# Performance work log

Measured on AMD Instinct MI355X. Metric: run time of the kernel, lower is better.

## Reference

```python
import jax, jax.numpy as jnp
import numpy as np

BATCH = 128
N = 4096
STEPNUM = 100
X = 10.0
DX = X / N               # grid spacing
BETA = 0.1
DT = 0.75 * DX / 1.5     # CFL-stable dt per module's update() rule (max|f'| ~ 1.5)


def _flux(u):
    # f_real with is_real=True:
    # f = 0.5*u*(3 - u^2) + beta/12 * u^2 * (3/4 - 2u + 3/2 u^2 - 1/4 u^4)
    u2 = u * u
    return 0.5 * u * (3.0 - u2) + (BETA / 12.0) * u2 * (0.75 - 2.0 * u + 1.5 * u2 - 0.25 * u2 * u2)


def _dflux(u):
    # analytic df/du (same value torch.autograd.grad computes in df_du)
    u2 = u * u
    u3 = u2 * u
    return 1.5 - 1.5 * u2 + (BETA / 12.0) * (1.5 * u - 6.0 * u2 + 6.0 * u3 - 1.5 * u2 * u3)


def setup_inputs() -> dict:
    key = jax.random.key(0)
    init = jax.random.uniform(key, (BATCH, N), dtype=jnp.float32)  # [B, N] in [0,1)
    return {"init": init, "stepnum": STEPNUM}


def reference(init, stepnum):
    r = jnp.float32(DT / DX)

    def step(u, _):
        f = _flux(u)                       # [B, N]
        a = jnp.abs(_dflux(u))             # [B, N], |f'(u)|
        # local Lax-Friedrichs speed: max over each adjacent pair (== torch.max over 2-slice)
        amax = jnp.maximum(a[:, :-1], a[:, 1:])                     # [B, N-1]
        f_half = 0.5 * (f[:, :-1] + f[:, 1:]) - 0.5 * amax * (u[:, 1:] - u[:, :-1])
        interior = u[:, 1:-1] - r * (f_half[:, 1:] - f_half[:, :-1])  # [B, N-2]
        # boundary copy: u[:,0]=u[:,1], u[:,N-1]=u[:,N-2]
        u_new = jnp.concatenate([interior[:, :1], interior, interior[:, -1:]], axis=1)
        return u_new, u_new

    _, traj = jax.lax.scan(step, init, None, length=stepnum - 1)  # [stepnum-1, B, N]
    return jnp.concatenate([init[None], traj], axis=0)           # [stepnum, B, N]
```

## Files before the change

### kernel.cpp

```cpp
#include <hip/hip_runtime.h>

#define BATCH 128
#define NPTS  4096
#define EPT   8
#define WREG  (64 * EPT)
#define HALOC 104
#define OWN   (WREG - 2 * HALOC)
#define SEGS  14
#define TPB   64

__device__ __forceinline__ void flux_eval(float u, float& g, float& ah) {
    constexpr float b  = 0.1f / 12.0f;
    constexpr float c6 = 0.5f * (-0.25f * b);
    constexpr float c4 = 0.5f * ( 1.5f  * b);
    constexpr float c3 = 0.5f * (-0.5f - 2.0f * b);
    constexpr float c2 = 0.5f * ( 0.75f * b);
    constexpr float c1 = 0.5f * ( 1.5f);
    constexpr float d5 = 0.5f * (-1.5f * b);
    constexpr float d3 = 0.5f * ( 6.0f * b);
    constexpr float d2 = 0.5f * (-(1.5f + 6.0f * b));
    constexpr float d1 = 0.5f * ( 1.5f * b);
    constexpr float d0 = 0.5f * ( 1.5f);

    float t = c6 * u;
    t = fmaf(t, u, c4);
    t = fmaf(t, u, c3);
    t = fmaf(t, u, c2);
    t = fmaf(t, u, c1);
    g = u * t;

    float e = d5 * u;
    e = fmaf(e, u, d3);
    e = fmaf(e, u, d2);
    e = fmaf(e, u, d1);
    e = fmaf(e, u, d0);
    ah = fabsf(e);
}

__global__ __launch_bounds__(TPB) void pde_wave_indep(
        const float* __restrict__ init,
        const int*   __restrict__ stepnum_p,
        float*       __restrict__ out) {
    const int wid  = blockIdx.x;
    const int lane = threadIdx.x;
    const int row  = wid / SEGS;
    const int seg  = wid - row * SEGS;

    const int ownlo = seg * OWN;
    const int base  = min(max(ownlo - HALOC, 0), NPTS - WREG);
    const int c0    = base + lane * EPT;
    const bool ownstore = (c0 >= ownlo) && (c0 < ownlo + OWN) && (c0 < NPTS);
    const bool bcL = (seg == 0) && (lane == 0);
    const bool bcR = (seg == SEGS - 1) && (lane == 63);
    const int stepnum = *stepnum_p;

    const float* ip = init + (size_t)row * NPTS + c0;
    const float4 A  = *(const float4*)ip;
    const float4 Bv = *(const float4*)(ip + 4);
    float v[EPT] = {A.x, A.y, A.z, A.w, Bv.x, Bv.y, Bv.z, Bv.w};

    float* op = out + (size_t)row * NPTS + c0;
    const size_t zstride = (size_t)BATCH * NPTS;

    if (ownstore) {
        *(float4*)op       = A;
        *(float4*)(op + 4) = Bv;
    }

    for (int s = 1; s < stepnum; ++s) {
        const float vl = __shfl_up(v[EPT - 1], 1, 64);
        const float vr = __shfl_down(v[0], 1, 64);

        float vv[EPT + 2];
        vv[0] = vl;
#pragma unroll
        for (int i = 0; i < EPT; ++i) vv[i + 1] = v[i];
        vv[EPT + 1] = vr;

        float g[EPT + 2], a[EPT + 2];
#pragma unroll
        for (int i = 0; i < EPT + 2; ++i) flux_eval(vv[i], g[i], a[i]);

        float fh[EPT + 1];
#pragma unroll
        for (int m = 0; m < EPT + 1; ++m)
            fh[m] = g[m] + g[m + 1] - fmaxf(a[m], a[m + 1]) * (vv[m + 1] - vv[m]);

#pragma unroll
        for (int i = 0; i < EPT; ++i)
            v[i] = fmaf(-0.5f, fh[i + 1] - fh[i], v[i]);

        if (bcL) v[0] = v[1];
        if (bcR) v[EPT - 1] = v[EPT - 2];

        op += zstride;
        if (ownstore) {
            *(float4*)op       = make_float4(v[0], v[1], v[2], v[3]);
            *(float4*)(op + 4) = make_float4(v[4], v[5], v[6], v[7]);
        }
    }
}

extern "C" void kernel_launch(void* const* d_in, const int* in_sizes, int n_in,
                              void* d_out, int out_size, void* d_ws, size_t ws_size,
                              hipStream_t stream) {
    const float* init  = (const float*)d_in[0];
    const int*   steps = (const int*)d_in[1];
    float*       out   = (float*)d_out;
    pde_wave_indep<<<BATCH * SEGS, TPB, 0, stream>>>(init, steps, out);
}
```

Measured before the change: 222.8 us.

## Temporally tile stencil with 4-cell register halos, exchanging every four steps

Each lane now keeps a 16-value window (8 owned cells plus 4 halo cells on each side) and advances four time steps per shuffle exchange, shrinking the updated range by one cell per step. Cross-lane shuffles drop from every step to every fourth step. In exchange, each lane recomputes redundant flux evaluations on the halo cells (14, 12, 10, 8 points across the four steps) and holds more registers. The main cost being attacked is shuffle latency and serialization in the per-step dependency chain.

```diff
diff --git a/kernel.cpp b/kernel.cpp
--- a/kernel.cpp
+++ b/kernel.cpp
@@ -3,6 +3,7 @@
 #define BATCH 128
 #define NPTS  4096
 #define EPT   8
+#define W     16
 #define WREG  (64 * EPT)
 #define HALOC 104
 #define OWN   (WREG - 2 * HALOC)
@@ -37,7 +38,42 @@
     ah = fabsf(e);
 }
 
-__global__ __launch_bounds__(TPB) void pde_wave_indep(
+template<int J>
+__device__ __forceinline__ void stepJ(float (&w)[W], const bool bcL, const bool bcR) {
+    constexpr int LO = J;
+    constexpr int HI = 15 - J;
+    constexpr int NS = HI - LO + 3;
+    float g[NS], a[NS];
+#pragma unroll
+    for (int i = 0; i < NS; ++i) flux_eval(w[LO - 1 + i], g[i], a[i]);
+    float fh[NS - 1];
+#pragma unroll
+    for (int m = 0; m < NS - 1; ++m)
+        fh[m] = g[m] + g[m + 1] - fmaxf(a[m], a[m + 1]) * (w[LO + m] - w[LO - 1 + m]);
+#pragma unroll
+    for (int i = LO; i <= HI; ++i)
+        w[i] = fmaf(-0.5f, fh[i - LO + 1] - fh[i - LO], w[i]);
+    if (bcL) w[4] = w[5];
+    if (bcR) w[11] = w[10];
+}
+
+__device__ __forceinline__ void exchange(float (&w)[W]) {
+    w[0]  = __shfl_up(w[8],  1, 64);
+    w[1]  = __shfl_up(w[9],  1, 64);
+    w[2]  = __shfl_up(w[10], 1, 64);
+    w[3]  = __shfl_up(w[11], 1, 64);
+    w[12] = __shfl_down(w[4], 1, 64);
+    w[13] = __shfl_down(w[5], 1, 64);
+    w[14] = __shfl_down(w[6], 1, 64);
+    w[15] = __shfl_down(w[7], 1, 64);
+}
+
+__device__ __forceinline__ void st_owned(float* p, const float (&w)[W]) {
+    *(float4*)p       = make_float4(w[4], w[5], w[6], w[7]);
+    *(float4*)(p + 4) = make_float4(w[8], w[9], w[10], w[11]);
+}
+
+__global__ __launch_bounds__(TPB) void pde_timetile(
         const float* __restrict__ init,
         const int*   __restrict__ stepnum_p,
         float*       __restrict__ out) {
@@ -49,55 +85,42 @@
     const int ownlo = seg * OWN;
     const int base  = min(max(ownlo - HALOC, 0), NPTS - WREG);
     const int c0    = base + lane * EPT;
-    const bool ownstore = (c0 >= ownlo) && (c0 < ownlo + OWN) && (c0 < NPTS);
+    const bool ownstore = (c0 >= ownlo) && (c0 < ownlo + OWN);
     const bool bcL = (seg == 0) && (lane == 0);
     const bool bcR = (seg == SEGS - 1) && (lane == 63);
     const int stepnum = *stepnum_p;
 
-    const float* ip = init + (size_t)row * NPTS + c0;
-    const float4 A  = *(const float4*)ip;
-    const float4 Bv = *(const float4*)(ip + 4);
-    float v[EPT] = {A.x, A.y, A.z, A.w, Bv.x, Bv.y, Bv.z, Bv.w};
+    const float* ip = init + (size_t)row * NPTS;
+    const int o0 = max(c0 - 4, 0);
+    const int o3 = min(c0 + 8, NPTS - 4);
+    const float4 L0 = *(const float4*)(ip + o0);
+    const float4 L1 = *(const float4*)(ip + c0);
+    const float4 L2 = *(const float4*)(ip + c0 + 4);
+    const float4 L3 = *(const float4*)(ip + o3);
+    float w[W] = {L0.x, L0.y, L0.z, L0.w, L1.x, L1.y, L1.z, L1.w,
+                  L2.x, L2.y, L2.z, L2.w, L3.x, L3.y, L3.z, L3.w};
 
+    const size_t Z = (size_t)BATCH * NPTS;
     float* op = out + (size_t)row * NPTS + c0;
-    const size_t zstride = (size_t)BATCH * NPTS;
 
-    if (ownstore) {
-        *(float4*)op       = A;
-        *(float4*)(op + 4) = Bv;
+    if (ownstore) st_owned(op, w);
+    op += Z;
+
+    int s = 1;
+    for (; s + 4 <= stepnum; s += 4) {
+        exchange(w);
+        stepJ<1>(w, bcL, bcR); if (ownstore) st_owned(op,         w);
+        stepJ<2>(w, bcL, bcR); if (ownstore) st_owned(op + Z,     w);
+        stepJ<3>(w, bcL, bcR); if (ownstore) st_owned(op + 2 * Z, w);
+        stepJ<4>(w, bcL, bcR); if (ownstore) st_owned(op + 3 * Z, w);
+        op += 4 * Z;
     }
-
-    for (int s = 1; s < stepnum; ++s) {
-        const float vl = __shfl_up(v[EPT - 1], 1, 64);
-        const float vr = __shfl_down(v[0], 1, 64);
-
-        float vv[EPT + 2];
-        vv[0] = vl;
-#pragma unroll
-        for (int i = 0; i < EPT; ++i) vv[i + 1] = v[i];
-        vv[EPT + 1] = vr;
-
-        float g[EPT + 2], a[EPT + 2];
-#pragma unroll
-        for (int i = 0; i < EPT + 2; ++i) flux_eval(vv[i], g[i], a[i]);
-
-        float fh[EPT + 1];
-#pragma unroll
-        for (int m = 0; m < EPT + 1; ++m)
-            fh[m] = g[m] + g[m + 1] - fmaxf(a[m], a[m + 1]) * (vv[m + 1] - vv[m]);
-
-#pragma unroll
-        for (int i = 0; i < EPT; ++i)
-            v[i] = fmaf(-0.5f, fh[i + 1] - fh[i], v[i]);
-
-        if (bcL) v[0] = v[1];
-        if (bcR) v[EPT - 1] = v[EPT - 2];
-
-        op += zstride;
-        if (ownstore) {
-            *(float4*)op       = make_float4(v[0], v[1], v[2], v[3]);
-            *(float4*)(op + 4) = make_float4(v[4], v[5], v[6], v[7]);
-        }
+    const int k = stepnum - s;
+    if (k > 0) {
+        exchange(w);
+        stepJ<1>(w, bcL, bcR); if (ownstore) st_owned(op, w);
+        if (k > 1) { stepJ<2>(w, bcL, bcR); if (ownstore) st_owned(op + Z, w); }
+        if (k > 2) { stepJ<3>(w, bcL, bcR); if (ownstore) st_owned(op + 2 * Z, w); }
     }
 }
 
@@ -107,5 +130,5 @@
     const float* init  = (const float*)d_in[0];
     const int*   steps = (const int*)d_in[1];
     float*       out   = (float*)d_out;
-    pde_wave_indep<<<BATCH * SEGS, TPB, 0, stream>>>(init, steps, out);
+    pde_timetile<<<BATCH * SEGS, TPB, 0, stream>>>(init, steps, out);
 }
```

Result: slower. 237.6 us (+6.6%).
